# Kernel optimization log

Measured on AMD Instinct MI355X. Metric: run time of the kernel, lower is better.

## Reference

```python
import jax, jax.numpy as jnp
import numpy as np

N = 10000   # nodes
E = 160000  # edges
D = 32      # hidden_dim == out_dim
IN = 2      # 'pos' node features
STEPS = 3   # GatedGraphConv n_steps


def setup_inputs() -> dict:
    key = jax.random.key(0)
    ks = jax.random.split(key, 16)
    s = 0.1  # init scale
    inp = {
        "x": jax.random.normal(ks[0], (N, IN), jnp.float32),
        "src": jax.random.randint(ks[1], (E,), 0, N, jnp.int64),
        "dst": jax.random.randint(ks[2], (E,), 0, N, jnp.int64),
        # node embedding Linear(in_dim, out_dim)
        "W_emb": jax.random.normal(ks[3], (IN, D), jnp.float32) * s,
        "b_emb": jnp.zeros((D,), jnp.float32),
        # EdgeConv: he = relu(theta(h_dst - h_src) + phi(h_src))
        "W_theta": jax.random.normal(ks[4], (D, D), jnp.float32) * s,
        "b_theta": jnp.zeros((D,), jnp.float32),
        "W_phi": jax.random.normal(ks[5], (D, D), jnp.float32) * s,
        "b_phi": jnp.zeros((D,), jnp.float32),
        # edge_func: Linear(D,64) -> ReLU -> Linear(64, D*D)
        "W1": jax.random.normal(ks[6], (D, 64), jnp.float32) * s,
        "b1": jnp.zeros((64,), jnp.float32),
        "W2": jax.random.normal(ks[7], (64, D * D), jnp.float32) * s,
        "b2": jnp.zeros((D * D,), jnp.float32),
        # GRUCell (torch convention), gates stacked [r|z|n]
        "W_ih": jax.random.normal(ks[8], (D, 3 * D), jnp.float32) * s,
        "b_ih": jnp.zeros((3 * D,), jnp.float32),
        "W_hh": jax.random.normal(ks[9], (D, 3 * D), jnp.float32) * s,
        "b_hh": jnp.zeros((3 * D,), jnp.float32),
    }
    return inp


def _gru_cell(a, h, W_ih, b_ih, W_hh, b_hh):
    gi = a @ W_ih + b_ih          # [N, 3D]
    gh = h @ W_hh + b_hh          # [N, 3D]
    i_r, i_z, i_n = jnp.split(gi, 3, axis=-1)
    h_r, h_z, h_n = jnp.split(gh, 3, axis=-1)
    r = jax.nn.sigmoid(i_r + h_r)
    z = jax.nn.sigmoid(i_z + h_z)
    n = jnp.tanh(i_n + r * h_n)
    return (1.0 - z) * n + z * h


def reference(x, src, dst, W_emb, b_emb, W_theta, b_theta, W_phi, b_phi,
              W1, b1, W2, b2, W_ih, b_ih, W_hh, b_hh):
    # node embedding
    h = x @ W_emb + b_emb                              # [N, D]
    # EdgeConv edge embedding (per edge)
    hs, hd = h[src], h[dst]                            # [E, D] gathers
    he = jax.nn.relu((hd - hs) @ W_theta + b_theta + hs @ W_phi + b_phi)  # [E, D]
    # NNConv-style per-edge weight matrices
    We = (jax.nn.relu(he @ W1 + b1) @ W2 + b2).reshape(E, D, D)           # [E, D, D]
    # gated (GRU) propagation for STEPS steps
    for _ in range(STEPS):
        msg = jnp.einsum('ei,eio->eo', h[src], We)     # per-edge gather-bmm
        a = jax.ops.segment_sum(msg, dst, num_segments=N)  # scatter-add [N, D]
        h = _gru_cell(a, h, W_ih, b_ih, W_hh, b_hh)
    return h
```

## Files before the change

### kernel.cpp

```cpp
#include <hip/hip_runtime.h>
#include <hip/hip_bf16.h>

#define D 32

typedef const float* fp;
typedef unsigned short u16;
typedef unsigned int u32;

using short8 = __attribute__((ext_vector_type(8))) short;
using f32x4  = __attribute__((ext_vector_type(4))) float;

__device__ __forceinline__ float b2f(u32 lo16) { return __uint_as_float(lo16 << 16); }
__device__ __forceinline__ u16 f2b(float f) {
    u32 x = __float_as_uint(f);
    return (u16)((x + 0x7fffu + ((x >> 16) & 1u)) >> 16);
}

__global__ void k_hev(fp x, fp W_emb, fp b_emb, fp Wth, fp bth, fp Wph, fp bph,
                      float* __restrict__ h, u16* __restrict__ hbf,
                      float* __restrict__ u, float* __restrict__ v,
                      float* __restrict__ a, int* __restrict__ cnt,
                      int* __restrict__ cursor, int Npad, int N) {
    __shared__ float sP[192];
    int tid = threadIdx.x;
    if (tid < 32) {
        int o = tid;
        float au0 = 0.f, au1 = 0.f, cu = 0.f, av0 = 0.f, av1 = 0.f, cv = 0.f;
        for (int i = 0; i < D; ++i) {
            float wt = Wth[i * D + o];
            float wd = Wph[i * D + o] - wt;
            au0 += W_emb[i] * wt;
            au1 += W_emb[D + i] * wt;
            cu  += b_emb[i] * wt;
            av0 += W_emb[i] * wd;
            av1 += W_emb[D + i] * wd;
            cv  += b_emb[i] * wd;
        }
        sP[o]       = au0;
        sP[32 + o]  = au1;
        sP[64 + o]  = cu + bth[o] + bph[o];
        sP[96 + o]  = av0;
        sP[128 + o] = av1;
        sP[160 + o] = cv;
    }
    __syncthreads();
    int t = blockIdx.x * 256 + tid;
    if (t >= N * D) return;
    a[t] = 0.f;
    if (t < Npad) cnt[t] = 0;
    if (t < N) cursor[t] = 0;
    int n = t >> 5, o = t & 31;
    float x0 = x[2 * n], x1 = x[2 * n + 1];
    float hv = x0 * W_emb[o] + x1 * W_emb[D + o] + b_emb[o];
    h[t] = hv;
    hbf[t] = f2b(hv);
    u[t] = x0 * sP[o] + x1 * sP[32 + o] + sP[64 + o];
    v[t] = x0 * sP[96 + o] + x1 * sP[128 + o] + sP[160 + o];
}

__global__ void k_w2frag(fp W2, u16* __restrict__ W2f) {
    int idx = blockIdx.x * 256 + threadIdx.x;
    int T = idx >> 9, r = idx & 511, l = r >> 3, j = r & 7;
    int ko = T * 16 + (l & 15);
    int i = (l >> 4) * 8 + j;
    W2f[idx] = f2b(W2[(size_t)(ko >> 5) * 1024 + i * 32 + (ko & 31)]);
}

__global__ void k_count(const int* __restrict__ src, int* __restrict__ cnt, int E) {
    int e = blockIdx.x * 256 + threadIdx.x;
    if (e < E) atomicAdd(&cnt[src[e]], 1);
}

__global__ void k_scan(const int* __restrict__ cnt, int* __restrict__ roff,
                       int* __restrict__ toff, int N) {
    __shared__ int pe[1024], pt[1024];
    int t = threadIdx.x;
    int per = (N + 1023) / 1024;
    int begin = t * per, end = min(begin + per, N);
    int se = 0, st = 0;
    for (int i = begin; i < end; ++i) { int c = cnt[i]; se += c; st += (c + 15) >> 4; }
    pe[t] = se; pt[t] = st;
    __syncthreads();
    for (int off = 1; off < 1024; off <<= 1) {
        int ve = (t >= off) ? pe[t - off] : 0;
        int vt = (t >= off) ? pt[t - off] : 0;
        __syncthreads();
        pe[t] += ve; pt[t] += vt;
        __syncthreads();
    }
    int pre_e = (t == 0) ? 0 : pe[t - 1];
    int pre_t = (t == 0) ? 0 : pt[t - 1];
    for (int i = begin; i < end; ++i) {
        int c = cnt[i];
        roff[i] = pre_e; pre_e += c;
        toff[i] = pre_t; pre_t += (c + 15) >> 4;
    }
    if (t == 0) { roff[N] = pe[1023]; toff[N] = pt[1023]; }
}

__global__ void k_scatter(const int* __restrict__ src, const int* __restrict__ dst,
                          const int* __restrict__ roff, int* __restrict__ cursor,
                          int* __restrict__ ssrc, int* __restrict__ sdst, int E) {
    int e = blockIdx.x * 256 + threadIdx.x;
    if (e >= E) return;
    int s = src[e];
    int p = roff[s] + atomicAdd(&cursor[s], 1);
    ssrc[p] = s;
    sdst[p] = dst[e];
}

__global__ void k_tiles(const int* __restrict__ cnt, const int* __restrict__ roff,
                        const int* __restrict__ toff, int* __restrict__ tilS,
                        int* __restrict__ tilB, int N) {
    int s = blockIdx.x * 256 + threadIdx.x;
    if (s >= N) return;
    int deg = cnt[s];
    if (deg == 0) return;
    int base = toff[s], beg = roff[s];
    int nt = (deg + 15) >> 4;
    for (int t = 0; t < nt; ++t) { tilS[base + t] = s; tilB[base + t] = beg + 16 * t; }
}

__global__ __launch_bounds__(256)
void k_edge2(const float* __restrict__ u, const float* __restrict__ v,
             const int* __restrict__ ssrc, const int* __restrict__ sdst,
             fp W1, fp b1, u16* __restrict__ g, int E) {
    __shared__ float sW1[D * 64];
    __shared__ float sb1[64];
    __shared__ float she[8][D];
    for (int i = threadIdx.x; i < D * 64; i += 256) sW1[i] = W1[i];
    if (threadIdx.x < 64) sb1[threadIdx.x] = b1[threadIdx.x];
    __syncthreads();
    int sub = threadIdx.x >> 5, o = threadIdx.x & 31;
    const float2* w2p = (const float2*)sW1;
    for (int e0 = blockIdx.x * 8; e0 < E; e0 += gridDim.x * 8) {
        int e = e0 + sub;
        if (e < E) {
            int s = ssrc[e], d2 = sdst[e];
            she[sub][o] = fmaxf(u[(size_t)d2 * D + o] + v[(size_t)s * D + o], 0.f);
        }
        __syncthreads();
        if (e < E) {
            float a0 = sb1[2 * o], a1 = sb1[2 * o + 1];
            #pragma unroll
            for (int i = 0; i < D; ++i) {
                float hv = she[sub][i];
                float2 w = w2p[i * 32 + o];
                a0 += hv * w.x;
                a1 += hv * w.y;
            }
            ((u32*)g)[(size_t)e * 32 + o] =
                (u32)f2b(fmaxf(a0, 0.f)) | ((u32)f2b(fmaxf(a1, 0.f)) << 16);
        }
        __syncthreads();
    }
}

__global__ __launch_bounds__(256)
void k_B(const float* __restrict__ h, fp b2, float* __restrict__ B, int N) {
    __shared__ float sb2[1024];
    for (int i = threadIdx.x; i < 1024; i += 256) sb2[i] = b2[i];
    __syncthreads();
    int t = blockIdx.x * 256 + threadIdx.x;
    if (t >= N * D) return;
    int n = t >> 5, o = t & 31;
    const float4* hv = (const float4*)(h + (size_t)n * D);
    float acc = 0.f;
    #pragma unroll
    for (int i4 = 0; i4 < 8; ++i4) {
        float4 v = hv[i4];
        acc += v.x * sb2[(4 * i4) * 32 + o] + v.y * sb2[(4 * i4 + 1) * 32 + o]
             + v.z * sb2[(4 * i4 + 2) * 32 + o] + v.w * sb2[(4 * i4 + 3) * 32 + o];
    }
    B[t] = acc;
}

__global__ __launch_bounds__(512)
void k_msgf(const u16* __restrict__ hbf, const u16* __restrict__ W2f,
            const float* __restrict__ Bv, const u32* __restrict__ g32,
            const int* __restrict__ tilS, const int* __restrict__ tilB,
            const int* __restrict__ roff, const int* __restrict__ toff,
            const int* __restrict__ sdst, float* __restrict__ a, int N) {
    __shared__ u32 sfrag[16 * 1024];
    int s0 = blockIdx.x * 16;
    int w = threadIdx.x >> 6, lp = threadIdx.x & 63;

    {
        int arow = s0 + (lp & 15);
        if (arow >= N) arow = N - 1;
        short8 afrag = *(const short8*)(hbf + (size_t)arow * 32 + (lp >> 4) * 8);
        int rbase = (lp >> 4) * 4;
        #pragma unroll
        for (int mi = 0; mi < 4; ++mi) {
            int k = w * 8 + 2 * mi;
            int kh = k >> 5;
            int kp = k & 31;
            int lt = ((kp >> 3) << 4) | (lp & 15);
            int jp = (kp & 7) >> 1;
            #pragma unroll
            for (int ot = 0; ot < 2; ++ot) {
                int T = 2 * k + ot;
                short8 bA = *(const short8*)(W2f + (size_t)T * 512 + lp * 8);
                short8 bB = *(const short8*)(W2f + (size_t)(T + 2) * 512 + lp * 8);
                f32x4 ca{0.f,0.f,0.f,0.f}, cb{0.f,0.f,0.f,0.f};
                ca = __builtin_amdgcn_mfma_f32_16x16x32_bf16(afrag, bA, ca, 0, 0, 0);
                cb = __builtin_amdgcn_mfma_f32_16x16x32_bf16(afrag, bB, cb, 0, 0, 0);
                int idx = (((kh << 1) | ot) << 8) + lt * 4 + jp;
                #pragma unroll
                for (int r = 0; r < 4; ++r)
                    sfrag[((rbase + r) << 10) + idx] =
                        (u32)f2b(ca[r]) | ((u32)f2b(cb[r]) << 16);
            }
        }
    }
    __syncthreads();

    int tbeg = toff[s0];
    int tend = toff[min(s0 + 16, N)];
    int ti = tbeg + w;
    uint4 A0c = make_uint4(0,0,0,0), A1c = A0c;
    int sC = 0, begC = 0, endC = 0;
    if (ti < tend) {
        sC = tilS[ti]; begC = tilB[ti]; endC = roff[sC + 1];
        int er = begC + (lp & 15);
        if (er < endC) {
            const uint4* gp = (const uint4*)(g32 + (size_t)er * 32);
            A0c = gp[lp >> 4];
            A1c = gp[4 + (lp >> 4)];
        }
    }
    while (ti < tend) {
        int tn = ti + 8;
        uint4 A0n = make_uint4(0,0,0,0), A1n = A0n;
        int sN = 0, begN = 0, endN = 0;
        if (tn < tend) {
            sN = tilS[tn]; begN = tilB[tn]; endN = roff[sN + 1];
            int er = begN + (lp & 15);
            if (er < endN) {
                const uint4* gp = (const uint4*)(g32 + (size_t)er * 32);
                A0n = gp[lp >> 4];
                A1n = gp[4 + (lp >> 4)];
            }
        }
        {
            union { uint4 u; short8 v; } A0, A1;
            A0.u = A0c; A1.u = A1c;
            const u32* mb = sfrag + ((sC - s0) << 10);
            union { uint4 u; short8 v; } B00, B01, B10, B11;
            B00.u = *(const uint4*)(mb + lp * 4);
            B01.u = *(const uint4*)(mb + 256 + lp * 4);
            B10.u = *(const uint4*)(mb + 512 + lp * 4);
            B11.u = *(const uint4*)(mb + 768 + lp * 4);
            f32x4 c0{0.f,0.f,0.f,0.f}, c1{0.f,0.f,0.f,0.f};
            c0 = __builtin_amdgcn_mfma_f32_16x16x32_bf16(A0.v, B00.v, c0, 0, 0, 0);
            c0 = __builtin_amdgcn_mfma_f32_16x16x32_bf16(A1.v, B10.v, c0, 0, 0, 0);
            c1 = __builtin_amdgcn_mfma_f32_16x16x32_bf16(A0.v, B01.v, c1, 0, 0, 0);
            c1 = __builtin_amdgcn_mfma_f32_16x16x32_bf16(A1.v, B11.v, c1, 0, 0, 0);
            int oc = lp & 15;
            float Bs0 = Bv[(size_t)sC * 32 + oc];
            float Bs1 = Bv[(size_t)sC * 32 + 16 + oc];
            int rb = (lp >> 4) * 4;
            #pragma unroll
            for (int r = 0; r < 4; ++r) {
                int e = begC + rb + r;
                if (e < endC) {
                    int d = sdst[e];
                    atomicAdd(&a[(size_t)d * 32 + oc],      c0[r] + Bs0);
                    atomicAdd(&a[(size_t)d * 32 + 16 + oc], c1[r] + Bs1);
                }
            }
        }
        ti = tn; sC = sN; begC = begN; endC = endN; A0c = A0n; A1c = A1n;
    }
}

__global__ __launch_bounds__(256)
void k_gru(float* __restrict__ a, const float* __restrict__ h,
           fp W_ih, fp b_ih, fp W_hh, fp b_hh,
           float* __restrict__ hout, u16* __restrict__ hbf, int N) {
    __shared__ float sWi[D * 96], sWh[D * 96], sbi[96], sbh[96];
    __shared__ float sa[32][D], sh[32][D];
    for (int i = threadIdx.x; i < D * 96; i += 256) { sWi[i] = W_ih[i]; sWh[i] = W_hh[i]; }
    if (threadIdx.x < 96) { sbi[threadIdx.x] = b_ih[threadIdx.x]; sbh[threadIdx.x] = b_hh[threadIdx.x]; }
    int n0 = blockIdx.x * 32;
    for (int i = threadIdx.x; i < 32 * D; i += 256) {
        int n = n0 + (i >> 5);
        if (n < N) {
            size_t idx = (size_t)n * D + (i & 31);
            sa[i >> 5][i & 31] = a[idx];
            sh[i >> 5][i & 31] = h[idx];
            a[idx] = 0.f;
        }
    }
    __syncthreads();
    int o = threadIdx.x & 31;
    #pragma unroll
    for (int z = 0; z < 4; ++z) {
        int sub = (threadIdx.x >> 5) + z * 8;
        int n = n0 + sub;
        if (n >= N) continue;
        float ir = sbi[o], iz = sbi[D + o], in_ = sbi[2 * D + o];
        float hr = sbh[o], hz = sbh[D + o], hn = sbh[2 * D + o];
        #pragma unroll
        for (int i = 0; i < D; ++i) {
            float av = sa[sub][i], hv = sh[sub][i];
            ir += av * sWi[i * 96 + o];
            iz += av * sWi[i * 96 + D + o];
            in_ += av * sWi[i * 96 + 2 * D + o];
            hr += hv * sWh[i * 96 + o];
            hz += hv * sWh[i * 96 + D + o];
            hn += hv * sWh[i * 96 + 2 * D + o];
        }
        float r = 1.f / (1.f + __expf(-(ir + hr)));
        float zz = 1.f / (1.f + __expf(-(iz + hz)));
        float nn = tanhf(in_ + r * hn);
        float hv2 = (1.f - zz) * nn + zz * sh[sub][o];
        size_t idx = (size_t)n * D + o;
        hout[idx] = hv2;
        hbf[idx] = f2b(hv2);
    }
}

extern "C" void kernel_launch(void* const* d_in, const int* in_sizes, int n_in,
                              void* d_out, int out_size, void* d_ws, size_t ws_size,
                              hipStream_t stream) {
    fp x      = (fp)d_in[0];
    const int* src = (const int*)d_in[1];
    const int* dst = (const int*)d_in[2];
    fp W_emb  = (fp)d_in[3];
    fp b_emb  = (fp)d_in[4];
    fp W_th   = (fp)d_in[5];
    fp b_th   = (fp)d_in[6];
    fp W_ph   = (fp)d_in[7];
    fp b_ph   = (fp)d_in[8];
    fp W1     = (fp)d_in[9];
    fp b1     = (fp)d_in[10];
    fp W2     = (fp)d_in[11];
    fp b2     = (fp)d_in[12];
    fp W_ih   = (fp)d_in[13];
    fp b_ih   = (fp)d_in[14];
    fp W_hh   = (fp)d_in[15];
    fp b_hh   = (fp)d_in[16];

    const int N = in_sizes[0] / 2;
    const int E = in_sizes[1];
    const int Npad = N + 4 - (N % 4);
    const int maxTiles = N + (E + 15) / 16;

    float* a      = (float*)d_ws;
    int*   cnt    = (int*)(a + (size_t)N * D);
    int*   cursor = cnt + Npad;
    int*   roff   = cursor + N;
    int*   toff   = roff + Npad;
    int*   ssrc   = toff + Npad;
    int*   sdst   = ssrc + E;
    int*   tilS   = sdst + E;
    int*   tilB   = tilS + maxTiles;
    float* hA     = (float*)(tilB + maxTiles);
    float* hB     = hA + (size_t)N * D;
    u16*   g      = (u16*)(hB + (size_t)N * D);
    u16*   hbf    = g + (size_t)E * 64;
    u16*   W2f    = hbf + (size_t)N * D;
    float* u      = (float*)(W2f + 65536);
    float* v      = u + (size_t)N * D;
    float* B      = v + (size_t)N * D;

    int ndBlocks = (N * D + 255) / 256;
    int eBlocks  = (E + 255) / 256;
    int nBlocks  = (N + 255) / 256;

    k_hev<<<ndBlocks, 256, 0, stream>>>(x, W_emb, b_emb, W_th, b_th, W_ph, b_ph,
                                        hA, hbf, u, v, a, cnt, cursor, Npad, N);
    k_w2frag<<<256, 256, 0, stream>>>(W2, W2f);
    k_count<<<eBlocks, 256, 0, stream>>>(src, cnt, E);
    k_scan<<<1, 1024, 0, stream>>>(cnt, roff, toff, N);
    k_scatter<<<eBlocks, 256, 0, stream>>>(src, dst, roff, cursor, ssrc, sdst, E);
    k_tiles<<<nBlocks, 256, 0, stream>>>(cnt, roff, toff, tilS, tilB, N);
    k_edge2<<<2048, 256, 0, stream>>>(u, v, ssrc, sdst, W1, b1, g, E);

    int fBlocks = (N + 15) / 16;
    float* hc = hA;
    float* hn_ = hB;
    for (int step = 0; step < 3; ++step) {
        k_B<<<ndBlocks, 256, 0, stream>>>(hc, b2, B, N);
        k_msgf<<<fBlocks, 512, 0, stream>>>(hbf, W2f, B, (const u32*)g, tilS, tilB,
                                            roff, toff, sdst, a, N);
        float* dstbuf = (step == 2) ? (float*)d_out : hn_;
        k_gru<<<(N + 31) / 32, 256, 0, stream>>>(a, hc, W_ih, b_ih, W_hh, b_hh, dstbuf, hbf, N);
        float* t = hc; hc = hn_; hn_ = t;
    }
}
```

Baseline: 240.2 us.

## Fuse small setup and bias-projection kernels into neighbors to cut launches

Folds the W2 fragment conversion and the initial h·b2 projection into the embedding kernel, moves tile-list construction into the single-block scan, and computes the next step's B = h·b2 inside the GRU kernel. This removes k_w2frag, k_tiles and three k_B launches along with the extra reload of h that k_B needed. In exchange, the scan block now writes tile entries serially, and the GRU and embedding kernels take on extra shared memory and a further sync. The GRU also computes B on the final step even though it is unused there.

```diff
diff --git a/kernel.cpp b/kernel.cpp
--- a/kernel.cpp
+++ b/kernel.cpp
@@ -17,11 +17,15 @@
 }
 
 __global__ void k_hev(fp x, fp W_emb, fp b_emb, fp Wth, fp bth, fp Wph, fp bph,
+                      fp W2, u16* __restrict__ W2f, fp b2,
                       float* __restrict__ h, u16* __restrict__ hbf,
                       float* __restrict__ u, float* __restrict__ v,
-                      float* __restrict__ a, int* __restrict__ cnt,
-                      int* __restrict__ cursor, int Npad, int N) {
+                      float* __restrict__ B, float* __restrict__ a,
+                      int* __restrict__ cnt, int* __restrict__ cursor,
+                      int Npad, int N) {
     __shared__ float sP[192];
+    __shared__ float shh[8][D];
+    __shared__ float sb2[1024];
     int tid = threadIdx.x;
     if (tid < 32) {
         int o = tid;
@@ -43,27 +47,38 @@
         sP[128 + o] = av1;
         sP[160 + o] = cv;
     }
+    if (blockIdx.x < 256) {
+        int idx = blockIdx.x * 256 + tid;
+        int T = idx >> 9, r = idx & 511, l = r >> 3, j = r & 7;
+        int ko = T * 16 + (l & 15);
+        int i = (l >> 4) * 8 + j;
+        W2f[idx] = f2b(W2[(size_t)(ko >> 5) * 1024 + i * 32 + (ko & 31)]);
+    }
+    for (int i = tid; i < 1024; i += 256) sb2[i] = b2[i];
     __syncthreads();
     int t = blockIdx.x * 256 + tid;
-    if (t >= N * D) return;
-    a[t] = 0.f;
-    if (t < Npad) cnt[t] = 0;
-    if (t < N) cursor[t] = 0;
+    bool active = (t < N * D);
     int n = t >> 5, o = t & 31;
-    float x0 = x[2 * n], x1 = x[2 * n + 1];
-    float hv = x0 * W_emb[o] + x1 * W_emb[D + o] + b_emb[o];
-    h[t] = hv;
-    hbf[t] = f2b(hv);
-    u[t] = x0 * sP[o] + x1 * sP[32 + o] + sP[64 + o];
-    v[t] = x0 * sP[96 + o] + x1 * sP[128 + o] + sP[160 + o];
-}
-
-__global__ void k_w2frag(fp W2, u16* __restrict__ W2f) {
-    int idx = blockIdx.x * 256 + threadIdx.x;
-    int T = idx >> 9, r = idx & 511, l = r >> 3, j = r & 7;
-    int ko = T * 16 + (l & 15);
-    int i = (l >> 4) * 8 + j;
-    W2f[idx] = f2b(W2[(size_t)(ko >> 5) * 1024 + i * 32 + (ko & 31)]);
+    if (active) {
+        a[t] = 0.f;
+        if (t < Npad) cnt[t] = 0;
+        if (t < N) cursor[t] = 0;
+        float x0 = x[2 * n], x1 = x[2 * n + 1];
+        float hv = x0 * W_emb[o] + x1 * W_emb[D + o] + b_emb[o];
+        h[t] = hv;
+        hbf[t] = f2b(hv);
+        shh[tid >> 5][o] = hv;
+        u[t] = x0 * sP[o] + x1 * sP[32 + o] + sP[64 + o];
+        v[t] = x0 * sP[96 + o] + x1 * sP[128 + o] + sP[160 + o];
+    }
+    __syncthreads();
+    if (active) {
+        int lr = tid >> 5;
+        float acc = 0.f;
+        #pragma unroll 8
+        for (int i = 0; i < D; ++i) acc += shh[lr][i] * sb2[i * 32 + o];
+        B[t] = acc;
+    }
 }
 
 __global__ void k_count(const int* __restrict__ src, int* __restrict__ cnt, int E) {
@@ -72,7 +87,8 @@
 }
 
 __global__ void k_scan(const int* __restrict__ cnt, int* __restrict__ roff,
-                       int* __restrict__ toff, int N) {
+                       int* __restrict__ toff, int* __restrict__ tilS,
+                       int* __restrict__ tilB, int N) {
     __shared__ int pe[1024], pt[1024];
     int t = threadIdx.x;
     int per = (N + 1023) / 1024;
@@ -92,8 +108,12 @@
     int pre_t = (t == 0) ? 0 : pt[t - 1];
     for (int i = begin; i < end; ++i) {
         int c = cnt[i];
-        roff[i] = pre_e; pre_e += c;
-        toff[i] = pre_t; pre_t += (c + 15) >> 4;
+        roff[i] = pre_e;
+        toff[i] = pre_t;
+        int nt2 = (c + 15) >> 4;
+        for (int q = 0; q < nt2; ++q) { tilS[pre_t + q] = i; tilB[pre_t + q] = pre_e + 16 * q; }
+        pre_e += c;
+        pre_t += nt2;
     }
     if (t == 0) { roff[N] = pe[1023]; toff[N] = pt[1023]; }
 }
@@ -107,18 +127,6 @@
     int p = roff[s] + atomicAdd(&cursor[s], 1);
     ssrc[p] = s;
     sdst[p] = dst[e];
-}
-
-__global__ void k_tiles(const int* __restrict__ cnt, const int* __restrict__ roff,
-                        const int* __restrict__ toff, int* __restrict__ tilS,
-                        int* __restrict__ tilB, int N) {
-    int s = blockIdx.x * 256 + threadIdx.x;
-    if (s >= N) return;
-    int deg = cnt[s];
-    if (deg == 0) return;
-    int base = toff[s], beg = roff[s];
-    int nt = (deg + 15) >> 4;
-    for (int t = 0; t < nt; ++t) { tilS[base + t] = s; tilB[base + t] = beg + 16 * t; }
 }
 
 __global__ __launch_bounds__(256)
@@ -154,25 +162,6 @@
         }
         __syncthreads();
     }
-}
-
-__global__ __launch_bounds__(256)
-void k_B(const float* __restrict__ h, fp b2, float* __restrict__ B, int N) {
-    __shared__ float sb2[1024];
-    for (int i = threadIdx.x; i < 1024; i += 256) sb2[i] = b2[i];
-    __syncthreads();
-    int t = blockIdx.x * 256 + threadIdx.x;
-    if (t >= N * D) return;
-    int n = t >> 5, o = t & 31;
-    const float4* hv = (const float4*)(h + (size_t)n * D);
-    float acc = 0.f;
-    #pragma unroll
-    for (int i4 = 0; i4 < 8; ++i4) {
-        float4 v = hv[i4];
-        acc += v.x * sb2[(4 * i4) * 32 + o] + v.y * sb2[(4 * i4 + 1) * 32 + o]
-             + v.z * sb2[(4 * i4 + 2) * 32 + o] + v.w * sb2[(4 * i4 + 3) * 32 + o];
-    }
-    B[t] = acc;
 }
 
 __global__ __launch_bounds__(512)
@@ -276,11 +265,14 @@
 
 __global__ __launch_bounds__(256)
 void k_gru(float* __restrict__ a, const float* __restrict__ h,
-           fp W_ih, fp b_ih, fp W_hh, fp b_hh,
-           float* __restrict__ hout, u16* __restrict__ hbf, int N) {
+           fp W_ih, fp b_ih, fp W_hh, fp b_hh, fp b2,
+           float* __restrict__ hout, u16* __restrict__ hbf,
+           float* __restrict__ Bout, int N) {
     __shared__ float sWi[D * 96], sWh[D * 96], sbi[96], sbh[96];
     __shared__ float sa[32][D], sh[32][D];
+    __shared__ float sb2[1024];
     for (int i = threadIdx.x; i < D * 96; i += 256) { sWi[i] = W_ih[i]; sWh[i] = W_hh[i]; }
+    for (int i = threadIdx.x; i < 1024; i += 256) sb2[i] = b2[i];
     if (threadIdx.x < 96) { sbi[threadIdx.x] = b_ih[threadIdx.x]; sbh[threadIdx.x] = b_hh[threadIdx.x]; }
     int n0 = blockIdx.x * 32;
     for (int i = threadIdx.x; i < 32 * D; i += 256) {
@@ -318,6 +310,18 @@
         size_t idx = (size_t)n * D + o;
         hout[idx] = hv2;
         hbf[idx] = f2b(hv2);
+        sa[sub][o] = hv2;
+    }
+    __syncthreads();
+    #pragma unroll
+    for (int z = 0; z < 4; ++z) {
+        int sub = (threadIdx.x >> 5) + z * 8;
+        int n = n0 + sub;
+        if (n >= N) continue;
+        float acc = 0.f;
+        #pragma unroll 8
+        for (int i = 0; i < D; ++i) acc += sa[sub][i] * sb2[i * 32 + o];
+        Bout[(size_t)n * D + o] = acc;
     }
 }
 
@@ -367,26 +371,24 @@
 
     int ndBlocks = (N * D + 255) / 256;
     int eBlocks  = (E + 255) / 256;
-    int nBlocks  = (N + 255) / 256;
 
     k_hev<<<ndBlocks, 256, 0, stream>>>(x, W_emb, b_emb, W_th, b_th, W_ph, b_ph,
-                                        hA, hbf, u, v, a, cnt, cursor, Npad, N);
-    k_w2frag<<<256, 256, 0, stream>>>(W2, W2f);
+                                        W2, W2f, b2, hA, hbf, u, v, B,
+                                        a, cnt, cursor, Npad, N);
     k_count<<<eBlocks, 256, 0, stream>>>(src, cnt, E);
-    k_scan<<<1, 1024, 0, stream>>>(cnt, roff, toff, N);
+    k_scan<<<1, 1024, 0, stream>>>(cnt, roff, toff, tilS, tilB, N);
     k_scatter<<<eBlocks, 256, 0, stream>>>(src, dst, roff, cursor, ssrc, sdst, E);
-    k_tiles<<<nBlocks, 256, 0, stream>>>(cnt, roff, toff, tilS, tilB, N);
     k_edge2<<<2048, 256, 0, stream>>>(u, v, ssrc, sdst, W1, b1, g, E);
 
     int fBlocks = (N + 15) / 16;
     float* hc = hA;
     float* hn_ = hB;
     for (int step = 0; step < 3; ++step) {
-        k_B<<<ndBlocks, 256, 0, stream>>>(hc, b2, B, N);
         k_msgf<<<fBlocks, 512, 0, stream>>>(hbf, W2f, B, (const u32*)g, tilS, tilB,
                                             roff, toff, sdst, a, N);
         float* dstbuf = (step == 2) ? (float*)d_out : hn_;
-        k_gru<<<(N + 31) / 32, 256, 0, stream>>>(a, hc, W_ih, b_ih, W_hh, b_hh, dstbuf, hbf, N);
+        k_gru<<<(N + 31) / 32, 256, 0, stream>>>(a, hc, W_ih, b_ih, W_hh, b_hh, b2,
+                                                 dstbuf, hbf, B, N);
         float* t = hc; hc = hn_; hn_ = t;
     }
 }
```

Result: no change. 241.4 us (+0.5%).
